# Kernel optimization log

Hardware: AMD Instinct MI355X
Metric: run time of the kernel (lower is better)

Reference implementation:

```python
import math
import jax, jax.numpy as jnp
import numpy as np

B, L, D, H = 2, 2048, 1024, 16
HD = D // H  # head_size = 64


def setup_inputs() -> dict:
    key = jax.random.key(0)
    kx, kk, kq, kv, ko = jax.random.split(key, 5)
    scale = 1.0 / math.sqrt(D)
    return {
        "x": jax.random.normal(kx, (B, L, D), dtype=jnp.float32),
        "Wk": jax.random.normal(kk, (D, D), dtype=jnp.float32) * scale,
        "Wq": jax.random.normal(kq, (D, D), dtype=jnp.float32) * scale,
        "Wv": jax.random.normal(kv, (D, D), dtype=jnp.float32) * scale,
        "Wo": jax.random.normal(ko, (D, D), dtype=jnp.float32) * scale,
    }


def reference(x, Wk, Wq, Wv, Wo):
    # Projections (torch Linear without bias; weights pre-stored as [in, out])
    k = (x @ Wk).reshape(B, L, H, HD)
    q = (x @ Wq).reshape(B, L, H, HD)
    v = (x @ Wv).reshape(B, L, H, HD)
    # Per-head causal attention, vectorized over heads instead of python loop
    inv_sqrt_hd = 1.0 / math.sqrt(HD)
    scores = jnp.einsum("blhd,bmhd->bhlm", q, k) * inv_sqrt_hd  # [B,H,L,L]
    causal = jnp.tril(jnp.ones((L, L), dtype=bool))
    scores = jnp.where(causal, scores, -jnp.inf)
    probs = jax.nn.softmax(scores, axis=-1)
    # Dropout is identity in eval mode (reference baseline is deterministic)
    out = jnp.einsum("bhlm,bmhd->blhd", probs, v).reshape(B, L, D)
    return out @ Wo
```

## Files before the change

### kernel.cpp

```cpp
#include <hip/hip_runtime.h>
#include <cstdint>

#define B_ 2
#define L_ 2048
#define D_ 1024
#define H_ 16
#define HD_ 64
#define ML_ (B_ * L_)
#define S_ (3 * D_)
#define QK_LD 2048

typedef __bf16 bf16;
typedef __attribute__((ext_vector_type(4))) __bf16 bf16x4;
typedef __attribute__((ext_vector_type(8))) __bf16 bf16x8;
typedef __attribute__((ext_vector_type(4))) float f32x4;
typedef __attribute__((ext_vector_type(16))) float f32x16;

__device__ __forceinline__ f32x4 mfma_16x16x32(bf16x8 a, bf16x8 b, f32x4 c) {
    return __builtin_amdgcn_mfma_f32_16x16x32_bf16(a, b, c, 0, 0, 0);
}
__device__ __forceinline__ f32x16 mfma_32x32x16(bf16x8 a, bf16x8 b, f32x16 c) {
    return __builtin_amdgcn_mfma_f32_32x32x16_bf16(a, b, c, 0, 0, 0);
}

#define GLDS16(g, l)                                                              \
    __builtin_amdgcn_global_load_lds((const __attribute__((address_space(1))) void*)(g), \
                                     (__attribute__((address_space(3))) void*)(l), 16, 0, 0)

__global__ __launch_bounds__(256) void cast_x_kernel(const float* __restrict__ in,
                                                     bf16* __restrict__ out, int n4) {
    int i = blockIdx.x * blockDim.x + threadIdx.x;
    if (i >= n4) return;
    float4 v = reinterpret_cast<const float4*>(in)[i];
    bf16x4 o;
    o[0] = (bf16)v.x; o[1] = (bf16)v.y; o[2] = (bf16)v.z; o[3] = (bf16)v.w;
    reinterpret_cast<bf16x4*>(out)[i] = o;
}

__global__ __launch_bounds__(1024) void transpose_w4_kernel(const float* __restrict__ Wq,
                                                            const float* __restrict__ Wk,
                                                            const float* __restrict__ Wv,
                                                            const float* __restrict__ Wo,
                                                            bf16* __restrict__ Wc) {
    __shared__ float tile[32][33];
    const int z = blockIdx.z;
    const float* W = (z == 0) ? Wq : (z == 1) ? Wk : (z == 2) ? Wv : Wo;
    bf16* Wt = Wc + (size_t)z * D_ * D_;
    int n0 = blockIdx.x * 32, k0 = blockIdx.y * 32;
    int tx = threadIdx.x, ty = threadIdx.y;
    tile[ty][tx] = W[(size_t)(k0 + ty) * D_ + n0 + tx];
    __syncthreads();
    Wt[(size_t)(n0 + ty) * D_ + k0 + tx] = (bf16)tile[tx][ty];
}

template <typename OutT>
__global__ __launch_bounds__(256) void gemm128_kernel(const bf16* __restrict__ A,
                                                      const bf16* __restrict__ Bt,
                                                      OutT* __restrict__ C,
                                                      bf16* __restrict__ vt,
                                                      int M, int N, int K, int ldc) {
    __shared__ bf16 As[128][32];
    __shared__ bf16 Bs[128][32];
    const int nwg = gridDim.x;
    const int bid = (blockIdx.x & 7) * (nwg >> 3) + (blockIdx.x >> 3);
    const int nb = N >> 7;
    const int bm = bid / nb, bn = bid % nb;
    const int m0 = bm << 7, n0 = bn << 7;
    const int t = threadIdx.x;
    const int lane = t & 63;
    const int w = t >> 6;
    const int wm = w >> 1, wn = w & 1;
    const int fr = lane & 15, fk = (lane >> 4) << 3;
    const int srow = (w << 5) + (lane >> 2);
    const int scol = (lane & 3) << 3;

    f32x4 acc[4][4] = {};
    for (int k0 = 0; k0 < K; k0 += 32) {
        const bf16* ga0 = &A[(size_t)(m0 + srow) * K + k0 + scol];
        const bf16* ga1 = &A[(size_t)(m0 + srow + 16) * K + k0 + scol];
        const bf16* gb0 = &Bt[(size_t)(n0 + srow) * K + k0 + scol];
        const bf16* gb1 = &Bt[(size_t)(n0 + srow + 16) * K + k0 + scol];
        __syncthreads();
        GLDS16(ga0, &As[(w << 5)][0]);
        GLDS16(ga1, &As[(w << 5) + 16][0]);
        GLDS16(gb0, &Bs[(w << 5)][0]);
        GLDS16(gb1, &Bs[(w << 5) + 16][0]);
        __syncthreads();
        bf16x8 a[4], b[4];
#pragma unroll
        for (int mt = 0; mt < 4; ++mt)
            a[mt] = *reinterpret_cast<const bf16x8*>(&As[(wm << 6) + (mt << 4) + fr][fk]);
#pragma unroll
        for (int nt = 0; nt < 4; ++nt)
            b[nt] = *reinterpret_cast<const bf16x8*>(&Bs[(wn << 6) + (nt << 4) + fr][fk]);
#pragma unroll
        for (int mt = 0; mt < 4; ++mt)
#pragma unroll
            for (int nt = 0; nt < 4; ++nt)
                acc[mt][nt] = mfma_16x16x32(a[mt], b[nt], acc[mt][nt]);
    }
    const int col = lane & 15, rq = (lane >> 4) << 2;
    if (vt != nullptr && n0 >= 2048) {
#pragma unroll
        for (int mt = 0; mt < 4; ++mt)
#pragma unroll
            for (int nt = 0; nt < 4; ++nt) {
                int cc = n0 - 2048 + (wn << 6) + (nt << 4) + col;
                int rrb = m0 + (wm << 6) + (mt << 4) + rq;
                int bb = rrb >> 11, l = rrb & (L_ - 1);
                size_t vrow = ((size_t)bb * H_ + (cc >> 6)) * HD_ + (cc & 63);
                bf16x4 pk;
#pragma unroll
                for (int reg = 0; reg < 4; ++reg) pk[reg] = (bf16)acc[mt][nt][reg];
                *reinterpret_cast<bf16x4*>(&vt[vrow * L_ + l]) = pk;
            }
    } else {
#pragma unroll
        for (int mt = 0; mt < 4; ++mt)
#pragma unroll
            for (int nt = 0; nt < 4; ++nt)
#pragma unroll
                for (int reg = 0; reg < 4; ++reg) {
                    int rr = m0 + (wm << 6) + (mt << 4) + rq + reg;
                    int cc = n0 + (wn << 6) + (nt << 4) + col;
                    C[(size_t)rr * ldc + cc] = (OutT)acc[mt][nt][reg];
                }
    }
}

__global__ __launch_bounds__(512) void attn_kernel(const bf16* __restrict__ qk,
                                                   const bf16* __restrict__ vt,
                                                   bf16* __restrict__ O) {
    __shared__ float Mrg[4][34][64];
    __shared__ bf16 Olds[4][32][72];
    const int nbh = B_ * H_;
    const int g = (int)(blockIdx.x / nbh);
    const int qt = (g < 8) ? (15 - g) : (g - 8);
    const int bh = blockIdx.x % nbh;
    const int h = bh % H_, b = bh / H_;
    const int t = threadIdx.x, lane = t & 63, w = t >> 6;
    const int p = w >> 1, s = w & 1;
    const int li = lane & 31, hi = lane >> 5;
    const int qg0 = qt * 128 + p * 32;
    const int q_g = qg0 + li;

    const bf16* kbase = qk + (size_t)b * L_ * QK_LD + D_ + h * HD_;
    const bf16* vbase = vt + (size_t)bh * HD_ * L_;

    const bf16* qrow_p = qk + (size_t)(b * L_ + q_g) * QK_LD + h * HD_ + hi * 8;
    bf16x8 qB[4];
#pragma unroll
    for (int c = 0; c < 4; ++c) qB[c] = *reinterpret_cast<const bf16x8*>(qrow_p + c * 16);

    f32x16 ot0 = {}, ot1 = {};
    float mrun = -1e30f, lsum = 0.f;
    const float c1 = 0.18033688011112042f;

    const int nkb = (qg0 + 31) / 64 + 1;
    for (int kb = s; kb < nkb; kb += 2) {
        const int c0 = kb * 64;
        f32x16 st0 = {}, st1 = {};
        const bf16* kp0 = kbase + (size_t)(c0 + li) * QK_LD + hi * 8;
        const bf16* kp1 = kp0 + (size_t)32 * QK_LD;
#pragma unroll
        for (int c = 0; c < 4; ++c) {
            st0 = mfma_32x32x16(*reinterpret_cast<const bf16x8*>(kp0 + c * 16), qB[c], st0);
            st1 = mfma_32x32x16(*reinterpret_cast<const bf16x8*>(kp1 + c * 16), qB[c], st1);
        }
        if (c0 + 64 <= qg0) {
#pragma unroll
            for (int r = 0; r < 16; ++r) { st0[r] *= c1; st1[r] *= c1; }
        } else {
#pragma unroll
            for (int r = 0; r < 16; ++r) {
                const int kvl = (r & 3) + 8 * (r >> 2) + 4 * hi;
                st0[r] = (c0 + kvl <= q_g) ? st0[r] * c1 : -1e30f;
                st1[r] = (c0 + 32 + kvl <= q_g) ? st1[r] * c1 : -1e30f;
            }
        }
        float mx[16];
#pragma unroll
        for (int r = 0; r < 16; ++r) mx[r] = fmaxf(st0[r], st1[r]);
#pragma unroll
        for (int d = 8; d > 0; d >>= 1)
#pragma unroll
            for (int r = 0; r < d; ++r) mx[r] = fmaxf(mx[r], mx[r + d]);
        const float rm = fmaxf(mx[0], __shfl_xor(mx[0], 32));
        const float mn = fmaxf(mrun, rm);
        if (!__all(rm - mrun <= 8.0f)) {
            const float sc = exp2f(mrun - mn);
            lsum *= sc;
#pragma unroll
            for (int r = 0; r < 16; ++r) { ot0[r] *= sc; ot1[r] *= sc; }
            mrun = mn;
        }
        float sm[16];
#pragma unroll
        for (int r = 0; r < 16; ++r) {
            float p0 = exp2f(st0[r] - mrun);
            float p1 = exp2f(st1[r] - mrun);
            st0[r] = p0; st1[r] = p1;
            sm[r] = p0 + p1;
        }
#pragma unroll
        for (int d = 8; d > 0; d >>= 1)
#pragma unroll
            for (int r = 0; r < d; ++r) sm[r] += sm[r + d];
        lsum += sm[0] + __shfl_xor(sm[0], 32);
        uint32_t wa[8], wb[8], ea[8], eb[8];
#pragma unroll
        for (int k = 0; k < 8; ++k) {
            asm("v_cvt_pk_bf16_f32 %0, %1, %2" : "=v"(wa[k]) : "v"(st0[2 * k]), "v"(st0[2 * k + 1]));
            asm("v_cvt_pk_bf16_f32 %0, %1, %2" : "=v"(wb[k]) : "v"(st1[2 * k]), "v"(st1[2 * k + 1]));
        }
#pragma unroll
        for (int k = 0; k < 8; ++k) {
            ea[k] = (uint32_t)__shfl_xor((int)wa[k], 32);
            eb[k] = (uint32_t)__shfl_xor((int)wb[k], 32);
        }
        union U8 { uint32_t u[4]; bf16x8 v; };
        U8 pb[4];
        pb[0].u[0] = hi ? ea[2] : wa[0]; pb[0].u[1] = hi ? ea[3] : wa[1];
        pb[0].u[2] = hi ? wa[2] : ea[0]; pb[0].u[3] = hi ? wa[3] : ea[1];
        pb[1].u[0] = hi ? ea[6] : wa[4]; pb[1].u[1] = hi ? ea[7] : wa[5];
        pb[1].u[2] = hi ? wa[6] : ea[4]; pb[1].u[3] = hi ? wa[7] : ea[5];
        pb[2].u[0] = hi ? eb[2] : wb[0]; pb[2].u[1] = hi ? eb[3] : wb[1];
        pb[2].u[2] = hi ? wb[2] : eb[0]; pb[2].u[3] = hi ? wb[3] : eb[1];
        pb[3].u[0] = hi ? eb[6] : wb[4]; pb[3].u[1] = hi ? eb[7] : wb[5];
        pb[3].u[2] = hi ? wb[6] : eb[4]; pb[3].u[3] = hi ? wb[7] : eb[5];
        const bf16* vp0 = vbase + (size_t)li * L_ + c0 + hi * 8;
        const bf16* vp1 = vbase + (size_t)(32 + li) * L_ + c0 + hi * 8;
#pragma unroll
        for (int j = 0; j < 4; ++j) {
            ot0 = mfma_32x32x16(*reinterpret_cast<const bf16x8*>(vp0 + j * 16), pb[j].v, ot0);
            ot1 = mfma_32x32x16(*reinterpret_cast<const bf16x8*>(vp1 + j * 16), pb[j].v, ot1);
        }
    }
    if (s == 1) {
#pragma unroll
        for (int r = 0; r < 16; ++r) {
            Mrg[p][r][lane] = ot0[r];
            Mrg[p][16 + r][lane] = ot1[r];
        }
        Mrg[p][32][lane] = mrun;
        Mrg[p][33][lane] = lsum;
    }
    __syncthreads();
    if (s == 0) {
        const float m1 = Mrg[p][32][lane], l1 = Mrg[p][33][lane];
        const float M = fmaxf(mrun, m1);
        const float sc0 = exp2f(mrun - M), sc1 = exp2f(m1 - M);
        const float rinv = 1.0f / (lsum * sc0 + l1 * sc1);
        const float f0 = sc0 * rinv, f1 = sc1 * rinv;
#pragma unroll
        for (int r2 = 0; r2 < 8; ++r2) {
            const int hd0 = 2 * (r2 & 1) + 8 * (r2 >> 1) + 4 * hi;
            uint32_t u0, u1;
            float a0 = ot0[2 * r2] * f0 + Mrg[p][2 * r2][lane] * f1;
            float a1 = ot0[2 * r2 + 1] * f0 + Mrg[p][2 * r2 + 1][lane] * f1;
            float b0 = ot1[2 * r2] * f0 + Mrg[p][16 + 2 * r2][lane] * f1;
            float b1 = ot1[2 * r2 + 1] * f0 + Mrg[p][16 + 2 * r2 + 1][lane] * f1;
            asm("v_cvt_pk_bf16_f32 %0, %1, %2" : "=v"(u0) : "v"(a0), "v"(a1));
            asm("v_cvt_pk_bf16_f32 %0, %1, %2" : "=v"(u1) : "v"(b0), "v"(b1));
            *reinterpret_cast<uint32_t*>(&Olds[p][li][hd0]) = u0;
            *reinterpret_cast<uint32_t*>(&Olds[p][li][32 + hd0]) = u1;
        }
    }
    __syncthreads();
    if (s == 0) {
        const int qr = lane >> 1, half = lane & 1;
        const size_t orow =
            ((size_t)b * L_ + qt * 128 + p * 32 + qr) * D_ + h * HD_ + half * 32;
#pragma unroll
        for (int k = 0; k < 4; ++k) {
            bf16x8 vv = *reinterpret_cast<const bf16x8*>(&Olds[p][qr][half * 32 + k * 8]);
            *reinterpret_cast<bf16x8*>(&O[orow + k * 8]) = vv;
        }
    }
}

extern "C" void kernel_launch(void* const* d_in, const int* in_sizes, int n_in,
                              void* d_out, int out_size, void* d_ws, size_t ws_size,
                              hipStream_t stream) {
    const float* x = (const float*)d_in[0];
    const float* Wk = (const float*)d_in[1];
    const float* Wq = (const float*)d_in[2];
    const float* Wv = (const float*)d_in[3];
    const float* Wo = (const float*)d_in[4];
    float* out = (float*)d_out;

    char* p = (char*)d_ws;
    const size_t xsz = (size_t)ML_ * D_ * sizeof(bf16);
    const size_t wsz = (size_t)D_ * D_ * sizeof(bf16);
    bf16* xb = (bf16*)p;   p += xsz;
    bf16* Wc = (bf16*)p;   p += 4 * wsz;
    bf16* Wot = Wc + 3 * (size_t)D_ * D_;
    bf16* qkb = (bf16*)p;  p += (size_t)ML_ * QK_LD * sizeof(bf16);
    bf16* vtb = (bf16*)p;  p += xsz;
    bf16* ab = xb;

    const int n4 = ML_ * D_ / 4;
    cast_x_kernel<<<(n4 + 255) / 256, 256, 0, stream>>>(x, xb, n4);
    dim3 tb(32, 32);
    dim3 tg(D_ / 32, D_ / 32, 4);
    transpose_w4_kernel<<<tg, tb, 0, stream>>>(Wq, Wk, Wv, Wo, Wc);

    gemm128_kernel<bf16><<<(ML_ / 128) * (S_ / 128), 256, 0, stream>>>(
        xb, Wc, qkb, vtb, ML_, S_, D_, QK_LD);

    attn_kernel<<<B_ * H_ * (L_ / 128), 512, 0, stream>>>(qkb, vtb, ab);

    gemm128_kernel<float><<<(ML_ / 128) * (D_ / 128), 256, 0, stream>>>(
        ab, Wot, out, nullptr, ML_, D_, D_, D_);
}
```

Before: 235.9 us.

## Templatize GEMM with K=64 swizzled LDS tiles, smaller output-projection tile, and MFMA priority

The GEMM becomes a template over tile sizes. Each iteration stages K=64 slices in LDS using an XOR swizzle to avoid bank conflicts, which halves the number of barrier-separated iterations. The output projection switches to 128x64 tiles, doubling its workgroup count to fill more CUs. s_setprio hints are placed around MFMA blocks in both the GEMM and the attention kernel to favour matrix issue. The cost is a larger LDS footprint per workgroup and possibly lower occupancy.

```diff
diff --git a/kernel.cpp b/kernel.cpp
--- a/kernel.cpp
+++ b/kernel.cpp
@@ -53,60 +53,72 @@
     Wt[(size_t)(n0 + ty) * D_ + k0 + tx] = (bf16)tile[tx][ty];
 }
 
-template <typename OutT>
-__global__ __launch_bounds__(256) void gemm128_kernel(const bf16* __restrict__ A,
-                                                      const bf16* __restrict__ Bt,
-                                                      OutT* __restrict__ C,
-                                                      bf16* __restrict__ vt,
-                                                      int M, int N, int K, int ldc) {
-    __shared__ bf16 As[128][32];
-    __shared__ bf16 Bs[128][32];
+template <int BM, int BN, typename OutT, bool VTEPI>
+__global__ __launch_bounds__(256) void gemm_kernel(const bf16* __restrict__ A,
+                                                   const bf16* __restrict__ Bt,
+                                                   OutT* __restrict__ C,
+                                                   bf16* __restrict__ vt,
+                                                   int M, int N, int K, int ldc) {
+    constexpr int MT = BM / 32, NT = BN / 32;
+    constexpr int RPW = (BM + BN) / 4;
+    constexpr int NC = RPW / 8;
+    __shared__ bf16 As[BM][64];
+    __shared__ bf16 Bs[BN][64];
     const int nwg = gridDim.x;
     const int bid = (blockIdx.x & 7) * (nwg >> 3) + (blockIdx.x >> 3);
-    const int nb = N >> 7;
+    const int nb = N / BN;
     const int bm = bid / nb, bn = bid % nb;
-    const int m0 = bm << 7, n0 = bn << 7;
-    const int t = threadIdx.x;
-    const int lane = t & 63;
-    const int w = t >> 6;
+    const int m0 = bm * BM, n0 = bn * BN;
+    const int t = threadIdx.x, lane = t & 63, w = t >> 6;
     const int wm = w >> 1, wn = w & 1;
-    const int fr = lane & 15, fk = (lane >> 4) << 3;
-    const int srow = (w << 5) + (lane >> 2);
-    const int scol = (lane & 3) << 3;
-
-    f32x4 acc[4][4] = {};
-    for (int k0 = 0; k0 < K; k0 += 32) {
-        const bf16* ga0 = &A[(size_t)(m0 + srow) * K + k0 + scol];
-        const bf16* ga1 = &A[(size_t)(m0 + srow + 16) * K + k0 + scol];
-        const bf16* gb0 = &Bt[(size_t)(n0 + srow) * K + k0 + scol];
-        const bf16* gb1 = &Bt[(size_t)(n0 + srow + 16) * K + k0 + scol];
+    const int fr = lane & 15;
+    const int lr8 = lane >> 3, lu = lane & 7;
+
+    f32x4 acc[MT][NT] = {};
+    for (int k0 = 0; k0 < K; k0 += 64) {
         __syncthreads();
-        GLDS16(ga0, &As[(w << 5)][0]);
-        GLDS16(ga1, &As[(w << 5) + 16][0]);
-        GLDS16(gb0, &Bs[(w << 5)][0]);
-        GLDS16(gb1, &Bs[(w << 5) + 16][0]);
+#pragma unroll
+        for (int c = 0; c < NC; ++c) {
+            const int br = w * RPW + c * 8;
+            const int row = br + lr8;
+            const int logu = lu ^ (row & 7);
+            if (br < BM)
+                GLDS16(&A[(size_t)(m0 + row) * K + k0 + logu * 8], &As[br][0]);
+            else
+                GLDS16(&Bt[(size_t)(n0 + row - BM) * K + k0 + logu * 8], &Bs[br - BM][0]);
+        }
         __syncthreads();
-        bf16x8 a[4], b[4];
-#pragma unroll
-        for (int mt = 0; mt < 4; ++mt)
-            a[mt] = *reinterpret_cast<const bf16x8*>(&As[(wm << 6) + (mt << 4) + fr][fk]);
-#pragma unroll
-        for (int nt = 0; nt < 4; ++nt)
-            b[nt] = *reinterpret_cast<const bf16x8*>(&Bs[(wn << 6) + (nt << 4) + fr][fk]);
-#pragma unroll
-        for (int mt = 0; mt < 4; ++mt)
-#pragma unroll
-            for (int nt = 0; nt < 4; ++nt)
-                acc[mt][nt] = mfma_16x16x32(a[mt], b[nt], acc[mt][nt]);
+#pragma unroll
+        for (int kk = 0; kk < 2; ++kk) {
+            const int lu0 = kk * 4 + (lane >> 4);
+            bf16x8 a[MT], b[NT];
+#pragma unroll
+            for (int mt = 0; mt < MT; ++mt) {
+                const int r = wm * (BM / 2) + mt * 16 + fr;
+                a[mt] = *reinterpret_cast<const bf16x8*>(&As[r][(lu0 ^ (r & 7)) * 8]);
+            }
+#pragma unroll
+            for (int nt = 0; nt < NT; ++nt) {
+                const int r = wn * (BN / 2) + nt * 16 + fr;
+                b[nt] = *reinterpret_cast<const bf16x8*>(&Bs[r][(lu0 ^ (r & 7)) * 8]);
+            }
+            __builtin_amdgcn_s_setprio(1);
+#pragma unroll
+            for (int mt = 0; mt < MT; ++mt)
+#pragma unroll
+                for (int nt = 0; nt < NT; ++nt)
+                    acc[mt][nt] = mfma_16x16x32(a[mt], b[nt], acc[mt][nt]);
+            __builtin_amdgcn_s_setprio(0);
+        }
     }
     const int col = lane & 15, rq = (lane >> 4) << 2;
-    if (vt != nullptr && n0 >= 2048) {
-#pragma unroll
-        for (int mt = 0; mt < 4; ++mt)
-#pragma unroll
-            for (int nt = 0; nt < 4; ++nt) {
-                int cc = n0 - 2048 + (wn << 6) + (nt << 4) + col;
-                int rrb = m0 + (wm << 6) + (mt << 4) + rq;
+    if (VTEPI && vt != nullptr && n0 >= 2048) {
+#pragma unroll
+        for (int mt = 0; mt < MT; ++mt)
+#pragma unroll
+            for (int nt = 0; nt < NT; ++nt) {
+                int cc = n0 - 2048 + wn * (BN / 2) + nt * 16 + col;
+                int rrb = m0 + wm * (BM / 2) + mt * 16 + rq;
                 int bb = rrb >> 11, l = rrb & (L_ - 1);
                 size_t vrow = ((size_t)bb * H_ + (cc >> 6)) * HD_ + (cc & 63);
                 bf16x4 pk;
@@ -116,13 +128,13 @@
             }
     } else {
 #pragma unroll
-        for (int mt = 0; mt < 4; ++mt)
-#pragma unroll
-            for (int nt = 0; nt < 4; ++nt)
+        for (int mt = 0; mt < MT; ++mt)
+#pragma unroll
+            for (int nt = 0; nt < NT; ++nt)
 #pragma unroll
                 for (int reg = 0; reg < 4; ++reg) {
-                    int rr = m0 + (wm << 6) + (mt << 4) + rq + reg;
-                    int cc = n0 + (wn << 6) + (nt << 4) + col;
+                    int rr = m0 + wm * (BM / 2) + mt * 16 + rq + reg;
+                    int cc = n0 + wn * (BN / 2) + nt * 16 + col;
                     C[(size_t)rr * ldc + cc] = (OutT)acc[mt][nt][reg];
                 }
     }
@@ -162,11 +174,13 @@
         f32x16 st0 = {}, st1 = {};
         const bf16* kp0 = kbase + (size_t)(c0 + li) * QK_LD + hi * 8;
         const bf16* kp1 = kp0 + (size_t)32 * QK_LD;
+        __builtin_amdgcn_s_setprio(1);
 #pragma unroll
         for (int c = 0; c < 4; ++c) {
             st0 = mfma_32x32x16(*reinterpret_cast<const bf16x8*>(kp0 + c * 16), qB[c], st0);
             st1 = mfma_32x32x16(*reinterpret_cast<const bf16x8*>(kp1 + c * 16), qB[c], st1);
         }
+        __builtin_amdgcn_s_setprio(0);
         if (c0 + 64 <= qg0) {
 #pragma unroll
             for (int r = 0; r < 16; ++r) { st0[r] *= c1; st1[r] *= c1; }
@@ -230,11 +244,13 @@
         pb[3].u[2] = hi ? wb[6] : eb[4]; pb[3].u[3] = hi ? wb[7] : eb[5];
         const bf16* vp0 = vbase + (size_t)li * L_ + c0 + hi * 8;
         const bf16* vp1 = vbase + (size_t)(32 + li) * L_ + c0 + hi * 8;
+        __builtin_amdgcn_s_setprio(1);
 #pragma unroll
         for (int j = 0; j < 4; ++j) {
             ot0 = mfma_32x32x16(*reinterpret_cast<const bf16x8*>(vp0 + j * 16), pb[j].v, ot0);
             ot1 = mfma_32x32x16(*reinterpret_cast<const bf16x8*>(vp1 + j * 16), pb[j].v, ot1);
         }
+        __builtin_amdgcn_s_setprio(0);
     }
     if (s == 1) {
 #pragma unroll
@@ -305,11 +321,11 @@
     dim3 tg(D_ / 32, D_ / 32, 4);
     transpose_w4_kernel<<<tg, tb, 0, stream>>>(Wq, Wk, Wv, Wo, Wc);
 
-    gemm128_kernel<bf16><<<(ML_ / 128) * (S_ / 128), 256, 0, stream>>>(
+    gemm_kernel<128, 128, bf16, true><<<(ML_ / 128) * (S_ / 128), 256, 0, stream>>>(
         xb, Wc, qkb, vtb, ML_, S_, D_, QK_LD);
 
     attn_kernel<<<B_ * H_ * (L_ / 128), 512, 0, stream>>>(qkb, vtb, ab);
 
-    gemm128_kernel<float><<<(ML_ / 128) * (D_ / 128), 256, 0, stream>>>(
+    gemm_kernel<128, 64, float, false><<<(ML_ / 128) * (D_ / 64), 256, 0, stream>>>(
         ab, Wot, out, nullptr, ML_, D_, D_, D_);
 }
```

Measured after the change: 221.1 us. 6.3% less time.
